# Performance work log

Hardware: AMD Instinct MI355X
Metric: run time of the kernel (lower is better)

## Reference

```python
import jax, jax.numpy as jnp
import numpy as np

N_Q = 32      # questions per batch
N_DOCS = 8    # docs per question (positive first)
Q_LEN = 32    # query tokens
D_LEN = 200   # doc tokens
DIM = 128     # ColBERT embedding dim


def setup_inputs() -> dict:
    key = jax.random.key(0)
    k1, k2 = jax.random.split(key)
    hq = jax.random.normal(k1, (N_Q, Q_LEN, DIM), dtype=jnp.float32)
    hd = jax.random.normal(k2, (N_Q * N_DOCS, D_LEN, DIM), dtype=jnp.float32)
    return {"hq": hq, "hd": hd}


def reference(hq, hd):
    # ColBERT maxsim: [n, m, q, d] token-level scores
    scores = jnp.einsum("nqh,mdh->nmqd", hq, hd)
    # max over doc tokens, mean over query tokens -> [n, m]
    score_matrix = jnp.max(scores, axis=-1).mean(axis=-1)

    n, m = score_matrix.shape
    n_docs = m // n
    # positive doc is the first in each group: targets = [0, n_docs, 2*n_docs, ...]
    targets = jnp.arange(0, m, n_docs)
    logp = jax.nn.log_softmax(score_matrix, axis=-1)
    loss = -jnp.mean(jnp.take_along_axis(logp, targets[:, None], axis=1))
    return score_matrix, loss
```

## Files before the change

kernel.cpp:

```cpp
#include <hip/hip_runtime.h>
#include <hip/hip_bf16.h>
#include <math.h>

typedef short short8 __attribute__((ext_vector_type(8)));
typedef float f32x4 __attribute__((ext_vector_type(4)));

#define NQ 32
#define NDOCS 8
#define QLEN 32
#define DLEN 200
#define DIM 128
#define MD 256
#define HD_ROWS 208
#define DOC_SHORTS (HD_ROWS * DIM)
#define DOC_BYTES (DOC_SHORTS * 2)
#define DOC_CHUNKS (HD_ROWS * 16)

__device__ __forceinline__ short f2bf(float x) {
    union { float f; unsigned u; } v; v.f = x;
    unsigned r = v.u + 0x7FFFu + ((v.u >> 16) & 1u);
    return (short)(r >> 16);
}

__device__ __forceinline__ short8 cvt8(float4 f0, float4 f1) {
    short8 o;
    o[0] = f2bf(f0.x); o[1] = f2bf(f0.y); o[2] = f2bf(f0.z); o[3] = f2bf(f0.w);
    o[4] = f2bf(f1.x); o[5] = f2bf(f1.y); o[6] = f2bf(f1.z); o[7] = f2bf(f1.w);
    return o;
}

__global__ __launch_bounds__(256) void convert_hd(const float* __restrict__ hd,
                                                  short* __restrict__ hdb) {
    unsigned c = blockIdx.x * 256 + threadIdx.x;
    unsigned m = c / DOC_CHUNKS;
    unsigned rc = c - m * DOC_CHUNKS;
    unsigned row = rc >> 4, kc = rc & 15;
    short8 o = {0, 0, 0, 0, 0, 0, 0, 0};
    if (row < DLEN) {
        const float4* p = reinterpret_cast<const float4*>(
            hd + ((size_t)m * DLEN + row) * DIM + kc * 8);
        o = cvt8(p[0], p[1]);
    }
    unsigned dst = m * DOC_CHUNKS + row * 16 + (kc ^ (row & 7));
    reinterpret_cast<short8*>(hdb)[dst] = o;
}

__global__ __launch_bounds__(512) void colbert_scores(const float* __restrict__ hq,
                                                      const short* __restrict__ hdb,
                                                      float* __restrict__ out) {
    __shared__ char lds[DOC_BYTES];
    const int tid = threadIdx.x;
    const int b = blockIdx.x;
    const int m = b & 255, qg = b >> 8;
    const int wid = tid >> 6, lane = tid & 63;
    const int lg = lane >> 4, lr = lane & 15;
    const int n = qg * 8 + wid;

    const char* gsrc = reinterpret_cast<const char*>(hdb + (size_t)m * DOC_SHORTS);
    {
        const int lbase = wid * 1024;
        const int gbase = lbase + lane * 16;
        #pragma unroll
        for (int i = 0; i < 6; ++i)
            __builtin_amdgcn_global_load_lds(
                (const __attribute__((address_space(1))) void*)(gsrc + i * 8192 + gbase),
                (__attribute__((address_space(3))) void*)(lds + i * 8192 + lbase),
                16, 0, 0);
        if (wid < 4)
            __builtin_amdgcn_global_load_lds(
                (const __attribute__((address_space(1))) void*)(gsrc + 49152 + gbase),
                (__attribute__((address_space(3))) void*)(lds + 49152 + lbase),
                16, 0, 0);
    }

    short8 Bq[2][4];
    #pragma unroll
    for (int qt = 0; qt < 2; ++qt)
        #pragma unroll
        for (int s = 0; s < 4; ++s) {
            const float4* p = reinterpret_cast<const float4*>(
                hq + (size_t)(n * QLEN + qt * 16 + lr) * DIM + s * 32 + lg * 8);
            Bq[qt][s] = cvt8(p[0], p[1]);
        }

    __syncthreads();

    int va[4];
    #pragma unroll
    for (int s = 0; s < 4; ++s)
        va[s] = lr * 256 + ((s * 64 + lg * 16) ^ ((lr & 7) << 4));

    float qmax0 = -INFINITY, qmax1 = -INFINITY;

#define STEP(DT, MASKED)                                                          \
    {                                                                             \
        f32x4 a0 = {0.f, 0.f, 0.f, 0.f}, a1 = {0.f, 0.f, 0.f, 0.f};               \
        _Pragma("unroll")                                                         \
        for (int s = 0; s < 4; ++s) {                                             \
            short8 A_ = *reinterpret_cast<const short8*>(&lds[va[s] + (DT) * 4096]); \
            a0 = __builtin_amdgcn_mfma_f32_16x16x32_bf16(A_, Bq[0][s], a0, 0, 0, 0); \
            a1 = __builtin_amdgcn_mfma_f32_16x16x32_bf16(A_, Bq[1][s], a1, 0, 0, 0); \
        }                                                                         \
        if (!(MASKED) || lg < 2) {                                                \
            qmax0 = fmaxf(qmax0, fmaxf(fmaxf(a0[0], a0[1]), fmaxf(a0[2], a0[3])));\
            qmax1 = fmaxf(qmax1, fmaxf(fmaxf(a1[0], a1[1]), fmaxf(a1[2], a1[3])));\
        }                                                                         \
    }

    #pragma unroll
    for (int dt = 0; dt < 12; ++dt) STEP(dt, false);
    STEP(12, true);
#undef STEP

    #pragma unroll
    for (int off = 16; off <= 32; off <<= 1) {
        qmax0 = fmaxf(qmax0, __shfl_xor(qmax0, off, 64));
        qmax1 = fmaxf(qmax1, __shfl_xor(qmax1, off, 64));
    }
    float s = qmax0 + qmax1;
    #pragma unroll
    for (int off = 1; off <= 8; off <<= 1) s += __shfl_xor(s, off, 64);
    if (lane == 0) out[(size_t)n * MD + m] = s * (1.0f / 32.0f);
}

__global__ __launch_bounds__(256) void colbert_loss(const float* __restrict__ scores,
                                                    float* __restrict__ loss_out) {
    __shared__ float terms[NQ];
    const int tid = threadIdx.x;
    const int wid = tid >> 6, lane = tid & 63;
    for (int n = wid; n < NQ; n += 4) {
        const float* row = scores + n * MD;
        float v0 = row[lane], v1 = row[64 + lane], v2 = row[128 + lane], v3 = row[192 + lane];
        float mx = fmaxf(fmaxf(v0, v1), fmaxf(v2, v3));
        #pragma unroll
        for (int off = 1; off < 64; off <<= 1) mx = fmaxf(mx, __shfl_xor(mx, off, 64));
        float s = expf(v0 - mx) + expf(v1 - mx) + expf(v2 - mx) + expf(v3 - mx);
        #pragma unroll
        for (int off = 1; off < 64; off <<= 1) s += __shfl_xor(s, off, 64);
        if (lane == 0) terms[n] = (mx + logf(s)) - row[n * NDOCS];
    }
    __syncthreads();
    if (tid == 0) {
        float acc = 0.f;
        #pragma unroll
        for (int n = 0; n < NQ; ++n) acc += terms[n];
        loss_out[0] = acc * (1.0f / NQ);
    }
}

extern "C" void kernel_launch(void* const* d_in, const int* in_sizes, int n_in,
                              void* d_out, int out_size, void* d_ws, size_t ws_size,
                              hipStream_t stream) {
    const float* hq = (const float*)d_in[0];
    const float* hd = (const float*)d_in[1];
    float* out = (float*)d_out;
    short* hdb = (short*)d_ws;

    convert_hd<<<3328, 256, 0, stream>>>(hd, hdb);
    colbert_scores<<<1024, 512, 0, stream>>>(hq, hdb, out);
    colbert_loss<<<1, 256, 0, stream>>>(out, out + NQ * MD);
}
```

Measured before the change: 43.37 us.

## Process two questions per wave to halve doc staging blocks

Each wave now handles two questions instead of one, so every block covers 16 questions per doc and the grid shrinks from 1024 to 512 blocks. Each doc tile is loaded into LDS half as often and every LDS A-fragment read feeds four MFMAs instead of two. The change also adds s_setprio around the MFMA bursts and a launch-bounds hint for two blocks per CU. In exchange it holds more registers for query fragments and accumulators and has fewer blocks to spread across CUs.

New measurement: 46.44 us. 7.1% more time.

```diff
diff --git a/kernel.cpp b/kernel.cpp
--- a/kernel.cpp
+++ b/kernel.cpp
@@ -45,16 +45,16 @@
     reinterpret_cast<short8*>(hdb)[dst] = o;
 }
 
-__global__ __launch_bounds__(512) void colbert_scores(const float* __restrict__ hq,
-                                                      const short* __restrict__ hdb,
-                                                      float* __restrict__ out) {
+__global__ __launch_bounds__(512, 2) void colbert_scores(const float* __restrict__ hq,
+                                                         const short* __restrict__ hdb,
+                                                         float* __restrict__ out) {
     __shared__ char lds[DOC_BYTES];
     const int tid = threadIdx.x;
     const int b = blockIdx.x;
-    const int m = b & 255, qg = b >> 8;
+    const int m = b & 255, qh = b >> 8;
     const int wid = tid >> 6, lane = tid & 63;
     const int lg = lane >> 4, lr = lane & 15;
-    const int n = qg * 8 + wid;
+    const int n0 = qh * 16 + wid * 2;
 
     const char* gsrc = reinterpret_cast<const char*>(hdb + (size_t)m * DOC_SHORTS);
     {
@@ -73,15 +73,17 @@
                 16, 0, 0);
     }
 
-    short8 Bq[2][4];
+    short8 Bq[2][2][4];
     #pragma unroll
-    for (int qt = 0; qt < 2; ++qt)
+    for (int nn = 0; nn < 2; ++nn)
         #pragma unroll
-        for (int s = 0; s < 4; ++s) {
-            const float4* p = reinterpret_cast<const float4*>(
-                hq + (size_t)(n * QLEN + qt * 16 + lr) * DIM + s * 32 + lg * 8);
-            Bq[qt][s] = cvt8(p[0], p[1]);
-        }
+        for (int qt = 0; qt < 2; ++qt)
+            #pragma unroll
+            for (int s = 0; s < 4; ++s) {
+                const float4* p = reinterpret_cast<const float4*>(
+                    hq + (size_t)((n0 + nn) * QLEN + qt * 16 + lr) * DIM + s * 32 + lg * 8);
+                Bq[nn][qt][s] = cvt8(p[0], p[1]);
+            }
 
     __syncthreads();
 
@@ -90,20 +92,30 @@
     for (int s = 0; s < 4; ++s)
         va[s] = lr * 256 + ((s * 64 + lg * 16) ^ ((lr & 7) << 4));
 
-    float qmax0 = -INFINITY, qmax1 = -INFINITY;
+    float qmax[2][2];
+    #pragma unroll
+    for (int nn = 0; nn < 2; ++nn)
+        #pragma unroll
+        for (int qt = 0; qt < 2; ++qt) qmax[nn][qt] = -INFINITY;
 
 #define STEP(DT, MASKED)                                                          \
     {                                                                             \
-        f32x4 a0 = {0.f, 0.f, 0.f, 0.f}, a1 = {0.f, 0.f, 0.f, 0.f};               \
+        f32x4 a00 = {0,0,0,0}, a01 = {0,0,0,0}, a10 = {0,0,0,0}, a11 = {0,0,0,0}; \
+        __builtin_amdgcn_s_setprio(1);                                            \
         _Pragma("unroll")                                                         \
         for (int s = 0; s < 4; ++s) {                                             \
             short8 A_ = *reinterpret_cast<const short8*>(&lds[va[s] + (DT) * 4096]); \
-            a0 = __builtin_amdgcn_mfma_f32_16x16x32_bf16(A_, Bq[0][s], a0, 0, 0, 0); \
-            a1 = __builtin_amdgcn_mfma_f32_16x16x32_bf16(A_, Bq[1][s], a1, 0, 0, 0); \
+            a00 = __builtin_amdgcn_mfma_f32_16x16x32_bf16(A_, Bq[0][0][s], a00, 0, 0, 0); \
+            a01 = __builtin_amdgcn_mfma_f32_16x16x32_bf16(A_, Bq[0][1][s], a01, 0, 0, 0); \
+            a10 = __builtin_amdgcn_mfma_f32_16x16x32_bf16(A_, Bq[1][0][s], a10, 0, 0, 0); \
+            a11 = __builtin_amdgcn_mfma_f32_16x16x32_bf16(A_, Bq[1][1][s], a11, 0, 0, 0); \
         }                                                                         \
+        __builtin_amdgcn_s_setprio(0);                                            \
         if (!(MASKED) || lg < 2) {                                                \
-            qmax0 = fmaxf(qmax0, fmaxf(fmaxf(a0[0], a0[1]), fmaxf(a0[2], a0[3])));\
-            qmax1 = fmaxf(qmax1, fmaxf(fmaxf(a1[0], a1[1]), fmaxf(a1[2], a1[3])));\
+            qmax[0][0] = fmaxf(qmax[0][0], fmaxf(fmaxf(a00[0], a00[1]), fmaxf(a00[2], a00[3]))); \
+            qmax[0][1] = fmaxf(qmax[0][1], fmaxf(fmaxf(a01[0], a01[1]), fmaxf(a01[2], a01[3]))); \
+            qmax[1][0] = fmaxf(qmax[1][0], fmaxf(fmaxf(a10[0], a10[1]), fmaxf(a10[2], a10[3]))); \
+            qmax[1][1] = fmaxf(qmax[1][1], fmaxf(fmaxf(a11[0], a11[1]), fmaxf(a11[2], a11[3]))); \
         }                                                                         \
     }
 
@@ -113,14 +125,24 @@
 #undef STEP
 
     #pragma unroll
-    for (int off = 16; off <= 32; off <<= 1) {
-        qmax0 = fmaxf(qmax0, __shfl_xor(qmax0, off, 64));
-        qmax1 = fmaxf(qmax1, __shfl_xor(qmax1, off, 64));
+    for (int off = 16; off <= 32; off <<= 1)
+        #pragma unroll
+        for (int nn = 0; nn < 2; ++nn)
+            #pragma unroll
+            for (int qt = 0; qt < 2; ++qt)
+                qmax[nn][qt] = fmaxf(qmax[nn][qt], __shfl_xor(qmax[nn][qt], off, 64));
+
+    float s0 = qmax[0][0] + qmax[0][1];
+    float s1 = qmax[1][0] + qmax[1][1];
+    #pragma unroll
+    for (int off = 1; off <= 8; off <<= 1) {
+        s0 += __shfl_xor(s0, off, 64);
+        s1 += __shfl_xor(s1, off, 64);
     }
-    float s = qmax0 + qmax1;
-    #pragma unroll
-    for (int off = 1; off <= 8; off <<= 1) s += __shfl_xor(s, off, 64);
-    if (lane == 0) out[(size_t)n * MD + m] = s * (1.0f / 32.0f);
+    if (lane == 0) {
+        out[(size_t)n0 * MD + m] = s0 * (1.0f / 32.0f);
+        out[(size_t)(n0 + 1) * MD + m] = s1 * (1.0f / 32.0f);
+    }
 }
 
 __global__ __launch_bounds__(256) void colbert_loss(const float* __restrict__ scores,
@@ -157,6 +179,6 @@
     short* hdb = (short*)d_ws;
 
     convert_hd<<<3328, 256, 0, stream>>>(hd, hdb);
-    colbert_scores<<<1024, 512, 0, stream>>>(hq, hdb, out);
+    colbert_scores<<<512, 512, 0, stream>>>(hq, hdb, out);
     colbert_loss<<<1, 256, 0, stream>>>(out, out + NQ * MD);
 }
```
